# Performance work log

Hardware: AMD Instinct MI355X
Metric: run time of the kernel (lower is better)

## Reference

```python
import jax, jax.numpy as jnp
import numpy as np

B, LA, LB = 16, 2048, 2048
DA, DB, DH = 768, 512, 512
EPS = 1e-5


def _layer_norm(x, g, b):
    mu = jnp.mean(x, axis=-1, keepdims=True)
    var = jnp.var(x, axis=-1, keepdims=True)
    return (x - mu) * jax.lax.rsqrt(var + EPS) * g + b


def setup_inputs() -> dict:
    key = jax.random.key(0)
    ks = jax.random.split(key, 12)
    s = lambda d: 1.0 / np.sqrt(d)
    return {
        "z_a": jax.random.normal(ks[0], (B, LA, DA), jnp.float32),
        "z_b": jax.random.normal(ks[1], (B, LB, DB), jnp.float32),
        "Wa": jax.random.uniform(ks[2], (DA, DH), jnp.float32, -s(DA), s(DA)),
        "ba": jnp.zeros((DH,), jnp.float32),
        "Wb": jax.random.uniform(ks[3], (DB, DH), jnp.float32, -s(DB), s(DB)),
        "bb": jnp.zeros((DH,), jnp.float32),
        "W_co": jax.random.normal(ks[4], (DH, DH), jnp.float32),
        "Woa": jax.random.uniform(ks[5], (DH, DA), jnp.float32, -s(DH), s(DH)),
        "boa": jnp.zeros((DA,), jnp.float32),
        "Wob": jax.random.uniform(ks[6], (DH, DB), jnp.float32, -s(DH), s(DH)),
        "bob": jnp.zeros((DB,), jnp.float32),
        "ga": jnp.ones((DA,), jnp.float32),
        "beta_a": jnp.zeros((DA,), jnp.float32),
        "gb": jnp.ones((DB,), jnp.float32),
        "beta_b": jnp.zeros((DB,), jnp.float32),
    }


def reference(z_a, z_b, Wa, ba, Wb, bb, W_co, Woa, boa, Wob, bob, ga, beta_a, gb, beta_b):
    # projections to shared hidden space
    h_a = jnp.einsum('bld,dh->blh', z_a, Wa) + ba          # (B, LA, DH)
    h_b = jnp.einsum('bld,dh->blh', z_b, Wb) + bb          # (B, LB, DH)
    # bilinear tanh co-attention scores
    C = jnp.tanh(jnp.einsum('bih,hk,bjk->bij', h_a, W_co, h_b))  # (B, LA, LB)
    attn_a = jax.nn.softmax(C, axis=-1)                    # rows: over LB
    attn_b = jax.nn.softmax(C.transpose(0, 2, 1), axis=-1) # cols: over LA
    h_a_co = jnp.einsum('bij,bjh->bih', attn_a, h_b)       # (B, LA, DH)
    h_b_co = jnp.einsum('bji,bih->bjh', attn_b, h_a)       # (B, LB, DH)
    z_a_co = jnp.einsum('blh,hd->bld', h_a_co, Woa) + boa
    z_b_co = jnp.einsum('blh,hd->bld', h_b_co, Wob) + bob
    z_a_out = _layer_norm(z_a + z_a_co, ga, beta_a)
    z_b_out = _layer_norm(z_b + z_b_co, gb, beta_b)
    return (z_a_out, z_b_out)
```

## Files before the change

kernel.cpp:

```cpp
#include <hip/hip_runtime.h>
#include <stdint.h>

typedef short bf16x8 __attribute__((ext_vector_type(8)));
typedef float f32x4 __attribute__((ext_vector_type(4)));

#define BM 128
#define BN 128
#define BK 64

#define AS1 __attribute__((address_space(1)))
#define AS3 __attribute__((address_space(3)))

__device__ __forceinline__ ushort f2bf(float x) {
    uint32_t u = __float_as_uint(x);
    u += 0x7FFFu + ((u >> 16) & 1u);
    return (ushort)(u >> 16);
}

__device__ __forceinline__ void gload16(const void* g, void* l) {
    __builtin_amdgcn_global_load_lds((const AS1 void*)g, (AS3 void*)l, 16, 0, 0);
}

template<int MODE, bool A_F32, bool HAS_BIAS, bool WRITE_T>
__global__ __launch_bounds__(256)
void gemm_bt(const void* __restrict__ Aptr_, const ushort* __restrict__ Bptr_,
             void* __restrict__ Cptr_, ushort* __restrict__ CTptr_,
             const float* __restrict__ bias, const float* __restrict__ resid_,
             float* __restrict__ rsum_, float* __restrict__ csum_,
             const float* __restrict__ scale_,
             int M, int N, int K, int lda, int ldb, int ldc,
             long sA, long sB, long sC, long sCT, long sSum,
             int ldct, int rbshift)
{
    __shared__ ushort Alds[BM * BK];
    __shared__ ushort Blds[BN * BK];

    const int z    = blockIdx.z;
    const int m0   = blockIdx.x * BM;
    const int n0   = blockIdx.y * BN;
    const int tid  = threadIdx.x;
    const int lane = tid & 63;
    const int wave = tid >> 6;
    const int wr   = wave >> 1, wc = wave & 1;
    const int g    = lane >> 4, c = lane & 15;

    const ushort* Bp = Bptr_ + z * sB;

    f32x4 acc[4][4] = {};

    for (int kt = 0; kt < K; kt += BK) {
        #pragma unroll
        for (int r = 0; r < 4; ++r) {
            const int li  = r * 256 + tid;
            const int row = li >> 3;
            const int ck  = li & 7;
            const int gck = ck ^ (row & 7);
            if constexpr (A_F32) {
                const float* src = (const float*)Aptr_ + z * sA + (long)(m0 + row) * lda + kt + gck * 8;
                const float4 f0 = *(const float4*)(src);
                const float4 f1 = *(const float4*)(src + 4);
                uint4 w;
                w.x = (uint)f2bf(f0.x) | ((uint)f2bf(f0.y) << 16);
                w.y = (uint)f2bf(f0.z) | ((uint)f2bf(f0.w) << 16);
                w.z = (uint)f2bf(f1.x) | ((uint)f2bf(f1.y) << 16);
                w.w = (uint)f2bf(f1.z) | ((uint)f2bf(f1.w) << 16);
                *(uint4*)&Alds[li * 8] = w;
            } else {
                const ushort* src = (const ushort*)Aptr_ + z * sA + (long)(m0 + row) * lda + kt + gck * 8;
                gload16(src, &Alds[li * 8]);
            }
            const ushort* srcb = Bp + (long)(n0 + row) * ldb + kt + gck * 8;
            gload16(srcb, &Blds[li * 8]);
        }
        __syncthreads();
        #pragma unroll
        for (int kk = 0; kk < 2; ++kk) {
            bf16x8 af[4], bfr[4];
            #pragma unroll
            for (int mi = 0; mi < 4; ++mi) {
                const int row = wr * 64 + mi * 16 + c;
                const int ckq = (kk * 4 + g) ^ (row & 7);
                af[mi] = *(const bf16x8*)&Alds[row * BK + ckq * 8];
            }
            #pragma unroll
            for (int ni = 0; ni < 4; ++ni) {
                const int row = wc * 64 + ni * 16 + c;
                const int ckq = (kk * 4 + g) ^ (row & 7);
                bfr[ni] = *(const bf16x8*)&Blds[row * BK + ckq * 8];
            }
            #pragma unroll
            for (int mi = 0; mi < 4; ++mi)
                #pragma unroll
                for (int ni = 0; ni < 4; ++ni)
                    acc[mi][ni] = __builtin_amdgcn_mfma_f32_16x16x32_bf16(af[mi], bfr[ni], acc[mi][ni], 0, 0, 0);
        }
        __syncthreads();
    }

    if constexpr (MODE == 0) {
        ushort* Cp = (ushort*)Cptr_ + z * sC;
        #pragma unroll
        for (int mi = 0; mi < 4; ++mi) {
            const int row = m0 + wr * 64 + mi * 16 + g * 4;
            #pragma unroll
            for (int ni = 0; ni < 4; ++ni) {
                const int col = n0 + wc * 64 + ni * 16 + c;
                const float bv = HAS_BIAS ? bias[col] : 0.f;
                ushort v[4];
                #pragma unroll
                for (int r = 0; r < 4; ++r) v[r] = f2bf(acc[mi][ni][r] + bv);
                #pragma unroll
                for (int r = 0; r < 4; ++r) Cp[(long)(row + r) * ldc + col] = v[r];
                if constexpr (WRITE_T) {
                    const int bb = row >> rbshift;
                    const int ii = row & ((1 << rbshift) - 1);
                    *(ushort4*)&CTptr_[(long)bb * sCT + (long)col * ldct + ii] =
                        make_ushort4(v[0], v[1], v[2], v[3]);
                }
            }
        }
    } else if constexpr (MODE == 1) {
        ushort* Ep  = (ushort*)Cptr_ + z * sC;
        ushort* ETp = CTptr_ + z * sCT;
        float* rs = rsum_ + z * sSum;
        float* cs = csum_ + z * sSum;
        float rowpart[4][4] = {};
        float colpart[4] = {};
        #pragma unroll
        for (int mi = 0; mi < 4; ++mi) {
            const int row = m0 + wr * 64 + mi * 16 + g * 4;
            #pragma unroll
            for (int ni = 0; ni < 4; ++ni) {
                const int col = n0 + wc * 64 + ni * 16 + c;
                ushort v[4];
                #pragma unroll
                for (int r = 0; r < 4; ++r) {
                    const float s = acc[mi][ni][r];
                    const float t = 1.f - 2.f / (__expf(2.f * s) + 1.f);
                    const float e = __expf(t);
                    rowpart[mi][r] += e;
                    colpart[ni]    += e;
                    v[r] = f2bf(e);
                }
                #pragma unroll
                for (int r = 0; r < 4; ++r) Ep[(long)(row + r) * ldc + col] = v[r];
                *(ushort4*)&ETp[(long)col * ldct + row] = make_ushort4(v[0], v[1], v[2], v[3]);
            }
        }
        #pragma unroll
        for (int mi = 0; mi < 4; ++mi) {
            #pragma unroll
            for (int r = 0; r < 4; ++r) {
                float v = rowpart[mi][r];
                v += __shfl_xor(v, 1); v += __shfl_xor(v, 2);
                v += __shfl_xor(v, 4); v += __shfl_xor(v, 8);
                if (c == 0) atomicAdd(&rs[m0 + wr * 64 + mi * 16 + g * 4 + r], v);
            }
        }
        #pragma unroll
        for (int ni = 0; ni < 4; ++ni) {
            float v = colpart[ni];
            v += __shfl_xor(v, 16); v += __shfl_xor(v, 32);
            if (g == 0) atomicAdd(&cs[n0 + wc * 64 + ni * 16 + c], v);
        }
    } else if constexpr (MODE == 2) {
        const float* sc = scale_ + z * sSum;
        ushort* Cp = (ushort*)Cptr_ + z * sC;
        #pragma unroll
        for (int mi = 0; mi < 4; ++mi) {
            const int row = m0 + wr * 64 + mi * 16 + g * 4;
            float rcp[4];
            #pragma unroll
            for (int r = 0; r < 4; ++r) rcp[r] = 1.f / sc[row + r];
            #pragma unroll
            for (int ni = 0; ni < 4; ++ni) {
                const int col = n0 + wc * 64 + ni * 16 + c;
                #pragma unroll
                for (int r = 0; r < 4; ++r)
                    Cp[(long)(row + r) * ldc + col] = f2bf(acc[mi][ni][r] * rcp[r]);
            }
        }
    } else {
        float* Co = (float*)Cptr_;
        #pragma unroll
        for (int mi = 0; mi < 4; ++mi) {
            const int row = m0 + wr * 64 + mi * 16 + g * 4;
            #pragma unroll
            for (int ni = 0; ni < 4; ++ni) {
                const int col = n0 + wc * 64 + ni * 16 + c;
                const float bv = bias[col];
                #pragma unroll
                for (int r = 0; r < 4; ++r) {
                    const long idx = (long)(row + r) * ldc + col;
                    Co[idx] = acc[mi][ni][r] + bv + resid_[idx];
                }
            }
        }
    }
}

__global__ __launch_bounds__(256)
void tcast(const float* __restrict__ in, ushort* __restrict__ out, int R, int C) {
    __shared__ float t[32][33];
    const int bx = blockIdx.x * 32, by = blockIdx.y * 32;
    const int tx = threadIdx.x, ty = threadIdx.y;
    for (int i = ty; i < 32; i += 8) {
        const int r = by + i, cc = bx + tx;
        if (r < R && cc < C) t[i][tx] = in[(long)r * C + cc];
    }
    __syncthreads();
    for (int i = ty; i < 32; i += 8) {
        const int cc = bx + i, r = by + tx;
        if (cc < C && r < R) out[(long)cc * R + r] = f2bf(t[tx][i]);
    }
}

template<int D>
__global__ __launch_bounds__(256)
void ln_rows(float* __restrict__ y, const float* __restrict__ gam, const float* __restrict__ bet) {
    constexpr int NV = D / 256;
    const long row = blockIdx.x;
    float* p = y + row * D;
    const int tid = threadIdx.x;
    float v[NV];
    float s = 0.f, s2 = 0.f;
    #pragma unroll
    for (int k = 0; k < NV; ++k) {
        v[k] = p[tid + k * 256];
        s += v[k]; s2 += v[k] * v[k];
    }
    #pragma unroll
    for (int off = 1; off < 64; off <<= 1) {
        s  += __shfl_xor(s, off);
        s2 += __shfl_xor(s2, off);
    }
    __shared__ float ws[4], ws2[4];
    const int wave = tid >> 6, lane = tid & 63;
    if (lane == 0) { ws[wave] = s; ws2[wave] = s2; }
    __syncthreads();
    s  = ws[0] + ws[1] + ws[2] + ws[3];
    s2 = ws2[0] + ws2[1] + ws2[2] + ws2[3];
    const float mu  = s / D;
    const float var = s2 / D - mu * mu;
    const float rstd = rsqrtf(var + 1e-5f);
    #pragma unroll
    for (int k = 0; k < NV; ++k) {
        const int i = tid + k * 256;
        p[i] = (v[k] - mu) * rstd * gam[i] + bet[i];
    }
}

extern "C" void kernel_launch(void* const* d_in, const int* in_sizes, int n_in,
                              void* d_out, int out_size, void* d_ws, size_t ws_size,
                              hipStream_t stream)
{
    (void)in_sizes; (void)n_in; (void)out_size; (void)ws_size;
    const float* z_a    = (const float*)d_in[0];
    const float* z_b    = (const float*)d_in[1];
    const float* Wa     = (const float*)d_in[2];
    const float* ba     = (const float*)d_in[3];
    const float* Wb     = (const float*)d_in[4];
    const float* bb     = (const float*)d_in[5];
    const float* Wco    = (const float*)d_in[6];
    const float* Woa    = (const float*)d_in[7];
    const float* boa    = (const float*)d_in[8];
    const float* Wob    = (const float*)d_in[9];
    const float* bob    = (const float*)d_in[10];
    const float* ga     = (const float*)d_in[11];
    const float* beta_a = (const float*)d_in[12];
    const float* gb     = (const float*)d_in[13];
    const float* beta_b = (const float*)d_in[14];

    const int Bn = 16, LA = 2048, LB = 2048, DA = 768, DB = 512, DH = 512;
    const long MA = (long)Bn * LA;
    const long MB = (long)Bn * LB;

    char* w = (char*)d_ws;
    size_t off = 0;
    auto alc = [&](size_t bytes) { void* p = w + off; off += (bytes + 255) & ~(size_t)255; return p; };

    ushort* WaT  = (ushort*)alc((size_t)DH * DA * 2);
    ushort* WbT  = (ushort*)alc((size_t)DH * DB * 2);
    ushort* WcoT = (ushort*)alc((size_t)DH * DH * 2);
    ushort* WoaT = (ushort*)alc((size_t)DA * DH * 2);
    ushort* WobT = (ushort*)alc((size_t)DB * DH * 2);
    ushort* h_a  = (ushort*)alc((size_t)MA * DH * 2);
    ushort* h_b  = (ushort*)alc((size_t)MB * DH * 2);
    ushort* h_aT = (ushort*)alc((size_t)Bn * DH * LA * 2);
    ushort* h_bT = (ushort*)alc((size_t)Bn * DH * LB * 2);
    ushort* Ma   = (ushort*)alc((size_t)MA * DH * 2);
    ushort* E    = (ushort*)alc((size_t)Bn * LA * LB * 2);
    ushort* ET   = (ushort*)alc((size_t)Bn * LB * LA * 2);
    ushort* Pa   = (ushort*)alc((size_t)MA * DH * 2);
    ushort* Pb   = (ushort*)alc((size_t)MB * DH * 2);
    float*  rsum = (float*)alc((size_t)Bn * LA * 4);
    float*  csum = (float*)alc((size_t)Bn * LB * 4);

    dim3 blk(256, 1, 1);
    dim3 tb(32, 8, 1);

    tcast<<<dim3(DH / 32, DA / 32, 1), tb, 0, stream>>>(Wa,  WaT,  DA, DH);
    tcast<<<dim3(DH / 32, DB / 32, 1), tb, 0, stream>>>(Wb,  WbT,  DB, DH);
    tcast<<<dim3(DH / 32, DH / 32, 1), tb, 0, stream>>>(Wco, WcoT, DH, DH);
    tcast<<<dim3(DA / 32, DH / 32, 1), tb, 0, stream>>>(Woa, WoaT, DH, DA);
    tcast<<<dim3(DB / 32, DH / 32, 1), tb, 0, stream>>>(Wob, WobT, DH, DB);

    hipMemsetAsync(rsum, 0, (size_t)Bn * (LA + LB) * sizeof(float), stream);

    gemm_bt<0, true, true, true><<<dim3(MA / BM, DH / BN, 1), blk, 0, stream>>>(
        z_a, WaT, h_a, h_aT, ba, nullptr, nullptr, nullptr, nullptr,
        (int)MA, DH, DA, DA, DA, DH, 0, 0, 0, (long)DH * LA, 0, LA, 11);

    gemm_bt<0, true, true, true><<<dim3(MB / BM, DH / BN, 1), blk, 0, stream>>>(
        z_b, WbT, h_b, h_bT, bb, nullptr, nullptr, nullptr, nullptr,
        (int)MB, DH, DB, DB, DB, DH, 0, 0, 0, (long)DH * LB, 0, LB, 11);

    gemm_bt<0, false, false, false><<<dim3(MA / BM, DH / BN, 1), blk, 0, stream>>>(
        h_a, WcoT, Ma, nullptr, nullptr, nullptr, nullptr, nullptr, nullptr,
        (int)MA, DH, DH, DH, DH, DH, 0, 0, 0, 0, 0, 0, 0);

    gemm_bt<1, false, false, false><<<dim3(LA / BM, LB / BN, Bn), blk, 0, stream>>>(
        Ma, h_b, E, ET, nullptr, nullptr, rsum, csum, nullptr,
        LA, LB, DH, DH, DH, LB,
        (long)LA * DH, (long)LB * DH, (long)LA * LB, (long)LB * LA, LA, LA, 0);

    gemm_bt<2, false, false, false><<<dim3(LA / BM, DH / BN, Bn), blk, 0, stream>>>(
        E, h_bT, Pa, nullptr, nullptr, nullptr, nullptr, nullptr, rsum,
        LA, DH, LB, LB, LB, DH,
        (long)LA * LB, (long)DH * LB, (long)LA * DH, 0, LA, 0, 0);

    gemm_bt<2, false, false, false><<<dim3(LB / BM, DH / BN, Bn), blk, 0, stream>>>(
        ET, h_aT, Pb, nullptr, nullptr, nullptr, nullptr, nullptr, csum,
        LB, DH, LA, LA, LA, DH,
        (long)LB * LA, (long)DH * LA, (long)LB * DH, 0, LB, 0, 0);

    float* outA = (float*)d_out;
    float* outB = outA + MA * DA;

    gemm_bt<3, false, true, false><<<dim3(MA / BM, DA / BN, 1), blk, 0, stream>>>(
        Pa, WoaT, outA, nullptr, boa, z_a, nullptr, nullptr, nullptr,
        (int)MA, DA, DH, DH, DH, DA, 0, 0, 0, 0, 0, 0, 0);

    gemm_bt<3, false, true, false><<<dim3(MB / BM, DB / BN, 1), blk, 0, stream>>>(
        Pb, WobT, outB, nullptr, bob, z_b, nullptr, nullptr, nullptr,
        (int)MB, DB, DH, DH, DH, DB, 0, 0, 0, 0, 0, 0, 0);

    ln_rows<768><<<dim3((unsigned)MA, 1, 1), blk, 0, stream>>>(outA, ga, beta_a);
    ln_rows<512><<<dim3((unsigned)MB, 1, 1), blk, 0, stream>>>(outB, gb, beta_b);
}
```

Before: 808.5 us.

## Double-buffer GEMM LDS tiles and pre-cast fp32 inputs to bf16

The GEMM main loop now keeps two LDS buffers and issues the async global-to-LDS loads for the next K tile before computing on the current one. Raw vmcnt/lgkmcnt waits and barriers replace the plain __syncthreads pair. The fp32 input path inside the GEMM is removed: z_a and z_b are first converted to bf16 by a separate cast kernel that writes into the still-unused E buffer, so every GEMM can use direct LDS loads. This costs twice the LDS per block, which may reduce occupancy, plus an extra pass over the inputs.

```diff
diff --git a/kernel.cpp b/kernel.cpp
--- a/kernel.cpp
+++ b/kernel.cpp
@@ -21,9 +21,9 @@
     __builtin_amdgcn_global_load_lds((const AS1 void*)g, (AS3 void*)l, 16, 0, 0);
 }
 
-template<int MODE, bool A_F32, bool HAS_BIAS, bool WRITE_T>
+template<int MODE, bool HAS_BIAS, bool WRITE_T>
 __global__ __launch_bounds__(256)
-void gemm_bt(const void* __restrict__ Aptr_, const ushort* __restrict__ Bptr_,
+void gemm_bt(const ushort* __restrict__ Aptr_, const ushort* __restrict__ Bptr_,
              void* __restrict__ Cptr_, ushort* __restrict__ CTptr_,
              const float* __restrict__ bias, const float* __restrict__ resid_,
              float* __restrict__ rsum_, float* __restrict__ csum_,
@@ -32,8 +32,8 @@
              long sA, long sB, long sC, long sCT, long sSum,
              int ldct, int rbshift)
 {
-    __shared__ ushort Alds[BM * BK];
-    __shared__ ushort Blds[BN * BK];
+    __shared__ ushort Alds[2][BM * BK];
+    __shared__ ushort Blds[2][BN * BK];
 
     const int z    = blockIdx.z;
     const int m0   = blockIdx.x * BM;
@@ -44,35 +44,34 @@
     const int wr   = wave >> 1, wc = wave & 1;
     const int g    = lane >> 4, c = lane & 15;
 
+    const ushort* Ap = Aptr_ + z * sA;
     const ushort* Bp = Bptr_ + z * sB;
 
     f32x4 acc[4][4] = {};
 
-    for (int kt = 0; kt < K; kt += BK) {
+    auto stage = [&](int ktoff, int buf) {
         #pragma unroll
         for (int r = 0; r < 4; ++r) {
             const int li  = r * 256 + tid;
             const int row = li >> 3;
-            const int ck  = li & 7;
-            const int gck = ck ^ (row & 7);
-            if constexpr (A_F32) {
-                const float* src = (const float*)Aptr_ + z * sA + (long)(m0 + row) * lda + kt + gck * 8;
-                const float4 f0 = *(const float4*)(src);
-                const float4 f1 = *(const float4*)(src + 4);
-                uint4 w;
-                w.x = (uint)f2bf(f0.x) | ((uint)f2bf(f0.y) << 16);
-                w.y = (uint)f2bf(f0.z) | ((uint)f2bf(f0.w) << 16);
-                w.z = (uint)f2bf(f1.x) | ((uint)f2bf(f1.y) << 16);
-                w.w = (uint)f2bf(f1.z) | ((uint)f2bf(f1.w) << 16);
-                *(uint4*)&Alds[li * 8] = w;
-            } else {
-                const ushort* src = (const ushort*)Aptr_ + z * sA + (long)(m0 + row) * lda + kt + gck * 8;
-                gload16(src, &Alds[li * 8]);
-            }
-            const ushort* srcb = Bp + (long)(n0 + row) * ldb + kt + gck * 8;
-            gload16(srcb, &Blds[li * 8]);
-        }
-        __syncthreads();
+            const int gck = (li & 7) ^ (row & 7);
+            gload16(Ap + (long)(m0 + row) * lda + ktoff + gck * 8, &Alds[buf][li * 8]);
+            gload16(Bp + (long)(n0 + row) * ldb + ktoff + gck * 8, &Blds[buf][li * 8]);
+        }
+    };
+
+    const int nk = K / BK;
+    stage(0, 0);
+    int cur = 0;
+    for (int t = 0; t < nk; ++t) {
+        if (t + 1 < nk) {
+            stage((t + 1) * BK, cur ^ 1);
+            asm volatile("s_waitcnt vmcnt(8)" ::: "memory");
+        } else {
+            asm volatile("s_waitcnt vmcnt(0)" ::: "memory");
+        }
+        __builtin_amdgcn_s_barrier();
+
         #pragma unroll
         for (int kk = 0; kk < 2; ++kk) {
             bf16x8 af[4], bfr[4];
@@ -80,13 +79,13 @@
             for (int mi = 0; mi < 4; ++mi) {
                 const int row = wr * 64 + mi * 16 + c;
                 const int ckq = (kk * 4 + g) ^ (row & 7);
-                af[mi] = *(const bf16x8*)&Alds[row * BK + ckq * 8];
+                af[mi] = *(const bf16x8*)&Alds[cur][row * BK + ckq * 8];
             }
             #pragma unroll
             for (int ni = 0; ni < 4; ++ni) {
                 const int row = wc * 64 + ni * 16 + c;
                 const int ckq = (kk * 4 + g) ^ (row & 7);
-                bfr[ni] = *(const bf16x8*)&Blds[row * BK + ckq * 8];
+                bfr[ni] = *(const bf16x8*)&Blds[cur][row * BK + ckq * 8];
             }
             #pragma unroll
             for (int mi = 0; mi < 4; ++mi)
@@ -94,7 +93,10 @@
                 for (int ni = 0; ni < 4; ++ni)
                     acc[mi][ni] = __builtin_amdgcn_mfma_f32_16x16x32_bf16(af[mi], bfr[ni], acc[mi][ni], 0, 0, 0);
         }
-        __syncthreads();
+
+        asm volatile("s_waitcnt lgkmcnt(0)" ::: "memory");
+        __builtin_amdgcn_s_barrier();
+        cur ^= 1;
     }
 
     if constexpr (MODE == 0) {
@@ -196,6 +198,21 @@
                 }
             }
         }
+    }
+}
+
+__global__ __launch_bounds__(256)
+void cast32to16(const float* __restrict__ in, ushort* __restrict__ out, long n) {
+    const long stride = (long)gridDim.x * 256 * 8;
+    for (long i = ((long)blockIdx.x * 256 + threadIdx.x) * 8; i < n; i += stride) {
+        const float4 f0 = *(const float4*)(in + i);
+        const float4 f1 = *(const float4*)(in + i + 4);
+        uint4 w;
+        w.x = (uint)f2bf(f0.x) | ((uint)f2bf(f0.y) << 16);
+        w.y = (uint)f2bf(f0.z) | ((uint)f2bf(f0.w) << 16);
+        w.z = (uint)f2bf(f1.x) | ((uint)f2bf(f1.y) << 16);
+        w.w = (uint)f2bf(f1.z) | ((uint)f2bf(f1.w) << 16);
+        *(uint4*)(out + i) = w;
     }
 }
 
@@ -296,6 +313,9 @@
     float*  rsum = (float*)alc((size_t)Bn * LA * 4);
     float*  csum = (float*)alc((size_t)Bn * LB * 4);
 
+    ushort* za16 = E;
+    ushort* zb16 = E + (size_t)MA * DA;
+
     dim3 blk(256, 1, 1);
     dim3 tb(32, 8, 1);
 
@@ -305,31 +325,34 @@
     tcast<<<dim3(DA / 32, DH / 32, 1), tb, 0, stream>>>(Woa, WoaT, DH, DA);
     tcast<<<dim3(DB / 32, DH / 32, 1), tb, 0, stream>>>(Wob, WobT, DH, DB);
 
+    cast32to16<<<dim3(2048, 1, 1), blk, 0, stream>>>(z_a, za16, MA * DA);
+    cast32to16<<<dim3(2048, 1, 1), blk, 0, stream>>>(z_b, zb16, MB * DB);
+
     hipMemsetAsync(rsum, 0, (size_t)Bn * (LA + LB) * sizeof(float), stream);
 
-    gemm_bt<0, true, true, true><<<dim3(MA / BM, DH / BN, 1), blk, 0, stream>>>(
-        z_a, WaT, h_a, h_aT, ba, nullptr, nullptr, nullptr, nullptr,
+    gemm_bt<0, true, true><<<dim3(MA / BM, DH / BN, 1), blk, 0, stream>>>(
+        za16, WaT, h_a, h_aT, ba, nullptr, nullptr, nullptr, nullptr,
         (int)MA, DH, DA, DA, DA, DH, 0, 0, 0, (long)DH * LA, 0, LA, 11);
 
-    gemm_bt<0, true, true, true><<<dim3(MB / BM, DH / BN, 1), blk, 0, stream>>>(
-        z_b, WbT, h_b, h_bT, bb, nullptr, nullptr, nullptr, nullptr,
+    gemm_bt<0, true, true><<<dim3(MB / BM, DH / BN, 1), blk, 0, stream>>>(
+        zb16, WbT, h_b, h_bT, bb, nullptr, nullptr, nullptr, nullptr,
         (int)MB, DH, DB, DB, DB, DH, 0, 0, 0, (long)DH * LB, 0, LB, 11);
 
-    gemm_bt<0, false, false, false><<<dim3(MA / BM, DH / BN, 1), blk, 0, stream>>>(
+    gemm_bt<0, false, false><<<dim3(MA / BM, DH / BN, 1), blk, 0, stream>>>(
         h_a, WcoT, Ma, nullptr, nullptr, nullptr, nullptr, nullptr, nullptr,
         (int)MA, DH, DH, DH, DH, DH, 0, 0, 0, 0, 0, 0, 0);
 
-    gemm_bt<1, false, false, false><<<dim3(LA / BM, LB / BN, Bn), blk, 0, stream>>>(
+    gemm_bt<1, false, false><<<dim3(LA / BM, LB / BN, Bn), blk, 0, stream>>>(
         Ma, h_b, E, ET, nullptr, nullptr, rsum, csum, nullptr,
         LA, LB, DH, DH, DH, LB,
         (long)LA * DH, (long)LB * DH, (long)LA * LB, (long)LB * LA, LA, LA, 0);
 
-    gemm_bt<2, false, false, false><<<dim3(LA / BM, DH / BN, Bn), blk, 0, stream>>>(
+    gemm_bt<2, false, false><<<dim3(LA / BM, DH / BN, Bn), blk, 0, stream>>>(
         E, h_bT, Pa, nullptr, nullptr, nullptr, nullptr, nullptr, rsum,
         LA, DH, LB, LB, LB, DH,
         (long)LA * LB, (long)DH * LB, (long)LA * DH, 0, LA, 0, 0);
 
-    gemm_bt<2, false, false, false><<<dim3(LB / BM, DH / BN, Bn), blk, 0, stream>>>(
+    gemm_bt<2, false, false><<<dim3(LB / BM, DH / BN, Bn), blk, 0, stream>>>(
         ET, h_aT, Pb, nullptr, nullptr, nullptr, nullptr, nullptr, csum,
         LB, DH, LA, LA, LA, DH,
         (long)LB * LA, (long)DH * LA, (long)LB * DH, 0, LB, 0, 0);
@@ -337,11 +360,11 @@
     float* outA = (float*)d_out;
     float* outB = outA + MA * DA;
 
-    gemm_bt<3, false, true, false><<<dim3(MA / BM, DA / BN, 1), blk, 0, stream>>>(
+    gemm_bt<3, true, false><<<dim3(MA / BM, DA / BN, 1), blk, 0, stream>>>(
         Pa, WoaT, outA, nullptr, boa, z_a, nullptr, nullptr, nullptr,
         (int)MA, DA, DH, DH, DH, DA, 0, 0, 0, 0, 0, 0, 0);
 
-    gemm_bt<3, false, true, false><<<dim3(MB / BM, DB / BN, 1), blk, 0, stream>>>(
+    gemm_bt<3, true, false><<<dim3(MB / BM, DB / BN, 1), blk, 0, stream>>>(
         Pb, WobT, outB, nullptr, bob, z_b, nullptr, nullptr, nullptr,
         (int)MB, DB, DH, DH, DH, DB, 0, 0, 0, 0, 0, 0, 0);
 
```

New measurement: 811.9 us. No clear change (+0.4%).
